# Optimization experiments

Hardware: AMD Instinct MI355X
Metric: run time of the kernel (lower is better)

## Reference

```python
import jax, jax.numpy as jnp
import numpy as np

ATTN_MASK_VALUE = -1e10
HEADS, DIM_HEAD, WSZ = 8, 64, 512


def ln(x, scale, eps=1e-5):
    # haiku LayerNorm(create_scale=True, create_offset=False, axis=-1)
    m = x.mean(-1, keepdims=True)
    v = ((x - m) ** 2).mean(-1, keepdims=True)
    return (x - m) / jnp.sqrt(v + eps) * scale


def local_attn(x, ln_s, qkv_w, ow, ob):
    n, _ = x.shape
    w = n // WSZ
    xn = ln(x, ln_s)
    qkv = xn @ qkv_w                                   # [n, 3*h*d]
    q, k, v = jnp.split(qkv, 3, axis=-1)
    resh = lambda t: t.reshape(w, WSZ, HEADS, DIM_HEAD).transpose(2, 0, 1, 3)  # h w n d
    q, k, v = resh(q), resh(k), resh(v)
    def lookback(t):
        t = jnp.pad(t, ((0, 0), (1, 0), (0, 0), (0, 0)))
        return jnp.concatenate((t[:, :-1], t[:, 1:]), axis=2)  # h w 2*wsz d
    k, v = lookback(k), lookback(v)
    sim = jnp.einsum('hwid,hwjd->hwij', q, k) * (DIM_HEAD ** -0.5)
    mask = jnp.tril(jnp.ones((WSZ, 2 * WSZ), dtype=bool), WSZ)
    sim = jnp.where(mask, sim, ATTN_MASK_VALUE)
    attn = jax.nn.softmax(sim, axis=-1)
    out = jnp.einsum('hwij,hwjd->hwid', attn, v)
    out = out.transpose(1, 2, 0, 3).reshape(n, HEADS * DIM_HEAD)
    return out @ ow + ob


def feedforward(x, ln_s, w1, b1, w2, b2):
    xn = ln(x, ln_s)
    return jax.nn.gelu(xn @ w1 + b1) @ w2 + b2


def gmlp(x, ln_s, win, bin_, sln, sw, sb, sow, sob, pow_, pob):
    n = x.shape[0]
    xn = ln(x, ln_s)
    h = jax.nn.gelu(xn @ win + bin_)                   # [n, d_ff]
    xg, gate = jnp.split(h, 2, axis=-1)                # [n, d_ff/2] each
    gate = ln(gate, sln)
    wm = sw * jnp.tril(jnp.ones((n, n), dtype=sw.dtype))
    gate = jnp.einsum('nd,mn->md', gate, wm) + sb      # causal spatial gate
    s = (xg * gate) @ sow + sob
    return s @ pow_ + pob


def forward(tokens, embed, attn_ln, attn_qkv, attn_ow, attn_ob,
            ff_ln, ff_w1, ff_b1, ff_w2, ff_b2,
            g_ln, g_win, g_bin, g_sln, g_sw, g_sb, g_sow, g_sob, g_pow, g_pob,
            fin_ln, head_w, head_b):
    x = embed[tokens]                                  # [n, dim]

    def block(xc, p):
        xc = xc + local_attn(xc, p['al'], p['aq'], p['aw'], p['ab'])
        xc = xc + feedforward(xc, p['fl'], p['f1'], p['fb1'], p['f2'], p['fb2'])
        return xc, None

    attn_params = {'al': attn_ln, 'aq': attn_qkv, 'aw': attn_ow, 'ab': attn_ob,
                   'fl': ff_ln, 'f1': ff_w1, 'fb1': ff_b1, 'f2': ff_w2, 'fb2': ff_b2}
    x, _ = jax.lax.scan(block, x, attn_params)

    def gblock(xc, p):
        xc = xc + gmlp(xc, p['l'], p['wi'], p['bi'], p['sl'], p['sw'], p['sb'],
                       p['so'], p['sob'], p['po'], p['pob'])
        return xc, None

    g_params = {'l': g_ln, 'wi': g_win, 'bi': g_bin, 'sl': g_sln, 'sw': g_sw,
                'sb': g_sb, 'so': g_sow, 'sob': g_sob, 'po': g_pow, 'pob': g_pob}
    x, _ = jax.lax.scan(gblock, x, g_params)

    return ln(x, fin_ln) @ head_w + head_b             # [n, num_tokens]


def setup_inputs() -> dict:
    key = jax.random.key(0)
    ks = jax.random.split(key, 16)
    n, dim, dff, inner, depth, gdepth, vocab = 2048, 1024, 4096, 512, 6, 2, 32
    sc = 0.02
    eps_sgu = 0.001 / n
    return {
        'tokens': jax.random.randint(ks[0], (n,), 0, vocab),
        'embed': jax.random.normal(ks[1], (vocab, dim)) * sc,
        'attn_ln': jnp.ones((depth, dim)),
        'attn_qkv': jax.random.normal(ks[2], (depth, dim, 3 * inner)) * sc,
        'attn_ow': jax.random.normal(ks[3], (depth, inner, dim)) * sc,
        'attn_ob': jnp.zeros((depth, dim)),
        'ff_ln': jnp.ones((depth, dim)),
        'ff_w1': jax.random.normal(ks[4], (depth, dim, dff)) * sc,
        'ff_b1': jnp.zeros((depth, dff)),
        'ff_w2': jax.random.normal(ks[5], (depth, dff, dim)) * sc,
        'ff_b2': jnp.zeros((depth, dim)),
        'g_ln': jnp.ones((gdepth, dim)),
        'g_win': jax.random.normal(ks[6], (gdepth, dim, dff)) * sc,
        'g_bin': jnp.zeros((gdepth, dff)),
        'g_sln': jnp.ones((gdepth, dff // 2)),
        'g_sw': jax.random.uniform(ks[7], (gdepth, n, n), minval=-eps_sgu, maxval=eps_sgu),
        'g_sb': jnp.ones((gdepth, n, 1)),
        'g_sow': jax.random.normal(ks[8], (gdepth, dff // 2, dff // 2)) * sc,
        'g_sob': jnp.zeros((gdepth, dff // 2)),
        'g_pow': jax.random.normal(ks[9], (gdepth, dff // 2, dim)) * sc,
        'g_pob': jnp.zeros((gdepth, dim)),
        'fin_ln': jnp.ones((dim,)),
        'head_w': jax.random.normal(ks[10], (dim, vocab)) * sc,
        'head_b': jnp.zeros((vocab,)),
    }


def reference(tokens, embed, attn_ln, attn_qkv, attn_ow, attn_ob,
              ff_ln, ff_w1, ff_b1, ff_w2, ff_b2,
              g_ln, g_win, g_bin, g_sln, g_sw, g_sb, g_sow, g_sob, g_pow, g_pob,
              fin_ln, head_w, head_b):
    return forward(tokens, embed, attn_ln, attn_qkv, attn_ow, attn_ob,
                   ff_ln, ff_w1, ff_b1, ff_w2, ff_b2,
                   g_ln, g_win, g_bin, g_sln, g_sw, g_sb, g_sow, g_sob, g_pow, g_pob,
                   fin_ln, head_w, head_b)
```

## Files before the change

kernel.cpp:

```cpp
#include <hip/hip_runtime.h>
#include <hip/hip_bf16.h>
#include <math.h>

using bf16 = __hip_bfloat16;
typedef __bf16 bf16x8 __attribute__((ext_vector_type(8)));
typedef float f32x4 __attribute__((ext_vector_type(4)));

__device__ __forceinline__ float toF(float v) { return v; }
__device__ __forceinline__ float toF(bf16 v) { return __bfloat162float(v); }

__device__ __forceinline__ float gelu_f(float x) {
  float t = tanhf(0.7978845608028654f * (x + 0.044715f * x * x * x));
  return 0.5f * x * (1.0f + t);
}

__device__ __forceinline__ void gld_lds16(const bf16* g, bf16* l) {
  __builtin_amdgcn_global_load_lds(
      (const __attribute__((address_space(1))) void*)g,
      (__attribute__((address_space(3))) void*)l, 16, 0, 0);
}

__device__ __forceinline__ float block_sum(float v) {
  __shared__ float tmp[8];
  int lane = threadIdx.x & 63, w = threadIdx.x >> 6, nw = blockDim.x >> 6;
#pragma unroll
  for (int o = 32; o > 0; o >>= 1) v += __shfl_down(v, o, 64);
  __syncthreads();
  if (lane == 0) tmp[w] = v;
  __syncthreads();
  float r = 0.f;
  for (int i = 0; i < nw; ++i) r += tmp[i];
  return r;
}

__device__ __forceinline__ float block_max(float v) {
  __shared__ float tmp2[8];
  int lane = threadIdx.x & 63, w = threadIdx.x >> 6, nw = blockDim.x >> 6;
#pragma unroll
  for (int o = 32; o > 0; o >>= 1) v = fmaxf(v, __shfl_down(v, o, 64));
  __syncthreads();
  if (lane == 0) tmp2[w] = v;
  __syncthreads();
  float r = -1e30f;
  for (int i = 0; i < nw; ++i) r = fmaxf(r, tmp2[i]);
  return r;
}

template <int BM, int BN, int EPI, int BK, int DBUF>
__launch_bounds__((BM / 64) * (BN / 64) * 64)
__global__ void gemm_bt(const bf16* __restrict__ A, int lda, long sAzh, long sAzw,
                        const bf16* __restrict__ B, int ldb, long sBzh, long sBzw,
                        void* __restrict__ C, int ldc, long sCzh, long sCzw,
                        int M, int N, int K, int zdiv,
                        const float* __restrict__ bias,
                        const float* __restrict__ rowbias,
                        const bf16* __restrict__ mul, int ldmul,
                        float* __restrict__ resid, int trilskip,
                        int nxk, int kchunk) {
  constexpr int LBK = (BK == 64) ? 6 : 5;
  constexpr int WM = BM / 64, WN = BN / 64;
  constexpr int NT = WM * WN * 64;
  constexpr int ACH = (BM * BK) / (NT * 8);
  constexpr int BCH = (BN * BK) / (NT * 8);
  __shared__ __align__(16) bf16 As[(DBUF ? 2 : 1) * BM * BK];
  __shared__ __align__(16) bf16 Bs[(DBUF ? 2 : 1) * BN * BK];
  const int tid = threadIdx.x;
  const int wave = tid >> 6, lane = tid & 63;
  const int wm = wave / WN, wn = wave % WN;
  int bx = blockIdx.x, kc = 0;
  if (kchunk > 0) { kc = bx / nxk; bx -= kc * nxk; }
  const int m0 = blockIdx.y * BM, n0 = bx * BN;
  const int z = blockIdx.z;
  const int zh = z / zdiv, zw = z % zdiv;
  A += zh * sAzh + zw * sAzw;
  B += zh * sBzh + zw * sBzw;
  const long coff = zh * sCzh + zw * sCzw;

  f32x4 acc[4][4];
#pragma unroll
  for (int i = 0; i < 4; ++i)
#pragma unroll
    for (int j = 0; j < 4; ++j)
#pragma unroll
      for (int r = 0; r < 4; ++r) acc[i][j][r] = 0.0f;

  const int kbeg = (kchunk > 0) ? kc * kchunk : 0;
  int kend = K;
  if (kchunk > 0 && kbeg + kchunk < kend) kend = kbeg + kchunk;
  if (trilskip && m0 + BM < kend) kend = m0 + BM;
  const int lrow = lane & 15, lk = (lane >> 4) << 3;

  auto stage = [&](int sel, int k0) {
    bf16* Ad = As + sel * BM * BK;
    bf16* Bd = Bs + sel * BN * BK;
#pragma unroll
    for (int c = 0; c < ACH; ++c) {
      int e = (c * NT + tid) << 3;
      int r = e >> LBK, kk = e & (BK - 1);
      gld_lds16(A + (long)(m0 + r) * lda + (k0 + kk), Ad + e);
    }
#pragma unroll
    for (int c = 0; c < BCH; ++c) {
      int e = (c * NT + tid) << 3;
      int r = e >> LBK, kk = e & (BK - 1);
      gld_lds16(B + (long)(n0 + r) * ldb + (k0 + kk), Bd + e);
    }
  };
  auto zero_diag = [&](int sel, int k0) {
    bf16* Ad = As + sel * BM * BK;
#pragma unroll
    for (int c = 0; c < ACH; ++c) {
      int e = (c * NT + tid) << 3;
      int r = e >> LBK, kk = e & (BK - 1);
      int m = m0 + r;
#pragma unroll
      for (int q = 0; q < 8; ++q)
        if (k0 + kk + q > m) Ad[e + q] = __float2bfloat16(0.0f);
    }
  };
  auto compute = [&](int sel) {
    const bf16* Ad = As + sel * BM * BK;
    const bf16* Bd = Bs + sel * BN * BK;
#pragma unroll
    for (int kk2 = 0; kk2 < BK; kk2 += 32) {
      bf16x8 af[4], bg[4];
#pragma unroll
      for (int i = 0; i < 4; ++i)
        af[i] = *(const bf16x8*)(Ad + (wm * 64 + i * 16 + lrow) * BK + kk2 + lk);
#pragma unroll
      for (int j = 0; j < 4; ++j)
        bg[j] = *(const bf16x8*)(Bd + (wn * 64 + j * 16 + lrow) * BK + kk2 + lk);
#pragma unroll
      for (int i = 0; i < 4; ++i)
#pragma unroll
        for (int j = 0; j < 4; ++j)
          acc[i][j] = __builtin_amdgcn_mfma_f32_16x16x32_bf16(af[i], bg[j], acc[i][j], 0, 0, 0);
    }
  };

  if constexpr (DBUF) {
    int cur = 0;
    stage(0, kbeg);
    __syncthreads();
    for (int k0 = kbeg; k0 < kend; k0 += BK) {
      if (k0 + BK < kend) stage(cur ^ 1, k0 + BK);
      if (trilskip && (k0 + BK > m0)) { zero_diag(cur, k0); __syncthreads(); }
      compute(cur);
      __syncthreads();
      cur ^= 1;
    }
  } else {
    for (int k0 = kbeg; k0 < kend; k0 += BK) {
      stage(0, k0);
      __syncthreads();
      if (trilskip && (k0 + BK > m0)) { zero_diag(0, k0); __syncthreads(); }
      compute(0);
      __syncthreads();
    }
  }

  const int rbase = m0 + wm * 64 + ((lane >> 4) << 2);
  const int cbase = n0 + wn * 64 + (lane & 15);
#pragma unroll
  for (int i = 0; i < 4; ++i) {
#pragma unroll
    for (int j = 0; j < 4; ++j) {
#pragma unroll
      for (int r = 0; r < 4; ++r) {
        int row = rbase + i * 16 + r;
        int col = cbase + j * 16;
        float v = acc[i][j][r];
        long idx = coff + (long)row * ldc + col;
        if (EPI == 0) {
          if (bias) v += bias[col];
          ((bf16*)C)[idx] = __float2bfloat16(v);
        } else if (EPI == 2) {
          v += bias[col];
          ((bf16*)C)[idx] = __float2bfloat16(gelu_f(v));
        } else if (EPI == 3) {
          if (kchunk > 0) {
            if (kbeg == 0 && bias) v += bias[col];
            atomicAdd(&resid[idx], v);
          } else {
            if (bias) v += bias[col];
            resid[idx] += v;
          }
        } else if (EPI == 4) {
          v += rowbias[row];
          v *= __bfloat162float(mul[(long)row * ldmul + col]);
          ((bf16*)C)[idx] = __float2bfloat16(v);
        }
      }
    }
  }
}

__global__ void k_embed(const int* __restrict__ tokens, const float* __restrict__ embed,
                        float* __restrict__ x) {
  int t = blockIdx.x;
  int tok = tokens[t];
  for (int j = threadIdx.x; j < 1024; j += 256)
    x[(long)t * 1024 + j] = embed[(long)tok * 1024 + j];
}

template <typename TIN>
__global__ void k_ln(const TIN* __restrict__ in, int ldin, const float* __restrict__ scale,
                     bf16* __restrict__ out, int ldout, int C) {
  int row = blockIdx.x, tid = threadIdx.x;
  const TIN* p = in + (long)row * ldin;
  float loc[8];
  int nper = C >> 8;
  float s = 0.f;
  for (int c = 0; c < nper; ++c) {
    float v = toF(p[c * 256 + tid]);
    loc[c] = v;
    s += v;
  }
  s = block_sum(s);
  float mean = s / (float)C;
  float s2 = 0.f;
  for (int c = 0; c < nper; ++c) {
    float d = loc[c] - mean;
    s2 += d * d;
  }
  s2 = block_sum(s2);
  float inv = 1.0f / sqrtf(s2 / (float)C + 1e-5f);
  for (int c = 0; c < nper; ++c) {
    int j = c * 256 + tid;
    out[(long)row * ldout + j] = __float2bfloat16((loc[c] - mean) * inv * scale[j]);
  }
}

template <typename TIN>
__global__ void k_transpose(const TIN* __restrict__ in, int ldin, bf16* __restrict__ out,
                            int ldout, int rows, int cols) {
  __shared__ bf16 tile[32][33];
  int c0 = blockIdx.x * 32, r0 = blockIdx.y * 32;
  int tx = threadIdx.x & 31, ty = threadIdx.x >> 5;
#pragma unroll
  for (int j = 0; j < 32; j += 8)
    tile[ty + j][tx] = __float2bfloat16(toF(in[(long)(r0 + ty + j) * ldin + c0 + tx]));
  __syncthreads();
#pragma unroll
  for (int j = 0; j < 32; j += 8)
    out[(long)(c0 + ty + j) * ldout + r0 + tx] = tile[tx][ty + j];
}

__global__ void k_cast(const float* __restrict__ in, bf16* __restrict__ out, long n) {
  long i = (long)blockIdx.x * 256 + threadIdx.x;
  if (i < n) out[i] = __float2bfloat16(in[i]);
}

__global__ void k_zerof(float* __restrict__ p, long n) {
  long i = (long)blockIdx.x * 256 + threadIdx.x;
  if (i < n) p[i] = 0.0f;
}

__global__ void k_packk(const bf16* __restrict__ qkv, bf16* __restrict__ kpad) {
  int idx = blockIdx.x * 256 + threadIdx.x;
  int d = idx & 63, t = (idx >> 6) & 2047, h = idx >> 17;
  kpad[(long)h * 163840 + (512 + t) * 64 + d] = qkv[(long)t * 1536 + 512 + h * 64 + d];
}

__global__ void k_zeropad(bf16* __restrict__ kpad, bf16* __restrict__ vtpad) {
  int idx = blockIdx.x * 256 + threadIdx.x;
  bf16 z = __float2bfloat16(0.0f);
  if (idx < 262144) {
    int h = idx >> 15, off = idx & 32767;
    kpad[(long)h * 163840 + off] = z;
  } else {
    int i = idx - 262144;
    int f = i >> 9, j = i & 511;
    vtpad[(long)f * 2560 + j] = z;
  }
}

__global__ void k_softmax(bf16* __restrict__ SP) {
  int row = blockIdx.x;
  int i = row & 511;
  int limit = i + 513;
  bf16* s = SP + (long)row * 1024;
  int tid = threadIdx.x;
  float v[4];
  float mx = -1e30f;
#pragma unroll
  for (int c = 0; c < 4; ++c) {
    int j = c * 256 + tid;
    float xv = (j < limit) ? __bfloat162float(s[j]) * 0.125f : -1e30f;
    v[c] = xv;
    mx = fmaxf(mx, xv);
  }
  mx = block_max(mx);
  float sum = 0.f;
#pragma unroll
  for (int c = 0; c < 4; ++c) {
    float e = (v[c] <= -1e29f) ? 0.f : expf(v[c] - mx);
    v[c] = e;
    sum += e;
  }
  sum = block_sum(sum);
  float inv = 1.0f / sum;
#pragma unroll
  for (int c = 0; c < 4; ++c) {
    int j = c * 256 + tid;
    s[j] = __float2bfloat16(v[c] * inv);
  }
}

__global__ void k_head(const float* __restrict__ x, const float* __restrict__ sc,
                       const float* __restrict__ w, const float* __restrict__ b,
                       float* __restrict__ out) {
  int row = blockIdx.x, tid = threadIdx.x;
  __shared__ float xn[1024];
  const float* p = x + (long)row * 1024;
  float loc[4];
  float s = 0.f;
#pragma unroll
  for (int c = 0; c < 4; ++c) {
    float v = p[c * 256 + tid];
    loc[c] = v;
    s += v;
  }
  s = block_sum(s);
  float mean = s / 1024.f;
  float s2 = 0.f;
#pragma unroll
  for (int c = 0; c < 4; ++c) {
    float d = loc[c] - mean;
    s2 += d * d;
  }
  s2 = block_sum(s2);
  float inv = 1.0f / sqrtf(s2 / 1024.f + 1e-5f);
#pragma unroll
  for (int c = 0; c < 4; ++c) {
    int j = c * 256 + tid;
    xn[j] = (loc[c] - mean) * inv * sc[j];
  }
  __syncthreads();
  int t = tid & 31, sl = tid >> 5;
  float partial = 0.f;
  for (int kk = 0; kk < 128; ++kk) {
    int k = sl * 128 + kk;
    partial += xn[k] * w[k * 32 + t];
  }
  __shared__ float red[256];
  red[tid] = partial;
  __syncthreads();
  if (tid < 32) {
    float r = 0.f;
    for (int q = 0; q < 8; ++q) r += red[q * 32 + t];
    out[(long)row * 32 + t] = r + b[t];
  }
}

extern "C" void kernel_launch(void* const* d_in, const int* in_sizes, int n_in,
                              void* d_out, int out_size, void* d_ws, size_t ws_size,
                              hipStream_t stream) {
  (void)in_sizes; (void)n_in; (void)out_size; (void)ws_size;
  const int*   tokens   = (const int*)d_in[0];
  const float* embed    = (const float*)d_in[1];
  const float* attn_ln  = (const float*)d_in[2];
  const float* attn_qkv = (const float*)d_in[3];
  const float* attn_ow  = (const float*)d_in[4];
  const float* attn_ob  = (const float*)d_in[5];
  const float* ff_ln    = (const float*)d_in[6];
  const float* ff_w1    = (const float*)d_in[7];
  const float* ff_b1    = (const float*)d_in[8];
  const float* ff_w2    = (const float*)d_in[9];
  const float* ff_b2    = (const float*)d_in[10];
  const float* g_ln     = (const float*)d_in[11];
  const float* g_win    = (const float*)d_in[12];
  const float* g_bin    = (const float*)d_in[13];
  const float* g_sln    = (const float*)d_in[14];
  const float* g_sw     = (const float*)d_in[15];
  const float* g_sb     = (const float*)d_in[16];
  const float* g_sow    = (const float*)d_in[17];
  const float* g_sob    = (const float*)d_in[18];
  const float* g_pow    = (const float*)d_in[19];
  const float* g_pob    = (const float*)d_in[20];
  const float* fin_ln   = (const float*)d_in[21];
  const float* head_w   = (const float*)d_in[22];
  const float* head_b   = (const float*)d_in[23];

  char* ws = (char*)d_ws;
  float* x  = (float*)ws;
  bf16* xn  = (bf16*)(ws + 8388608);
  char* SC  = ws + 12582912;
  bf16* qkv   = (bf16*)SC;
  bf16* kpad  = (bf16*)(SC + 6291456);
  bf16* vtpad = (bf16*)(SC + 8912896);
  bf16* SP    = (bf16*)(SC + 11534336);
  bf16* att   = (bf16*)(SC + 45088768);
  bf16* h      = (bf16*)SC;
  bf16* gateLN = (bf16*)(SC + 16777216);
  bf16* gateT  = (bf16*)(SC + 25165824);
  bf16* prod   = (bf16*)(SC + 33554432);
  bf16* sbuf   = (bf16*)(SC + 41943040);
  bf16* W  = (bf16*)(ws + 62914560);
  bf16* W2 = (bf16*)(ws + 71303168);
  float* att_f32 = (float*)(ws + 71303168);

  k_embed<<<2048, 256, 0, stream>>>(tokens, embed, x);

  for (int L = 0; L < 6; ++L) {
    const float* qkvw = attn_qkv + (long)L * 1024 * 1536;
    const float* oww  = attn_ow + (long)L * 512 * 1024;
    const float* w1   = ff_w1 + (long)L * 1024 * 4096;
    const float* w2   = ff_w2 + (long)L * 4096 * 1024;

    k_ln<float><<<2048, 256, 0, stream>>>(x, 1024, attn_ln + L * 1024, xn, 1024, 1024);
    k_transpose<float><<<dim3(48, 32), 256, 0, stream>>>(qkvw, 1536, W, 1024, 1024, 1536);
    gemm_bt<128, 128, 0, 64, 1><<<dim3(12, 16, 1), 256, 0, stream>>>(
        xn, 1024, 0, 0, W, 1024, 0, 0, qkv, 1536, 0, 0,
        2048, 1536, 1024, 1, nullptr, nullptr, nullptr, 0, nullptr, 0, 0, 0);

    k_packk<<<4096, 256, 0, stream>>>(qkv, kpad);
    k_zeropad<<<2048, 256, 0, stream>>>(kpad, vtpad);
    k_transpose<bf16><<<dim3(16, 64), 256, 0, stream>>>(qkv + 1024, 1536, vtpad + 512, 2560, 2048, 512);

    gemm_bt<128, 128, 0, 64, 0><<<dim3(8, 4, 32), 256, 0, stream>>>(
        qkv, 1536, 64, 786432, kpad, 64, 163840, 32768, SP, 1024, 2097152, 524288,
        512, 1024, 64, 4, nullptr, nullptr, nullptr, 0, nullptr, 0, 0, 0);
    k_softmax<<<16384, 256, 0, stream>>>(SP);
    k_zerof<<<4096, 256, 0, stream>>>(att_f32, 1048576L);
    gemm_bt<128, 64, 3, 64, 1><<<dim3(4, 4, 32), 128, 0, stream>>>(
        SP, 1024, 2097152, 524288, vtpad, 2560, 163840, 512, nullptr, 512, 64, 262144,
        512, 64, 1024, 4, nullptr, nullptr, nullptr, 0, att_f32, 0, 1, 256);
    k_cast<<<4096, 256, 0, stream>>>(att_f32, att, 1048576L);
    k_transpose<float><<<dim3(32, 16), 256, 0, stream>>>(oww, 1024, W, 512, 512, 1024);
    gemm_bt<128, 128, 3, 64, 1><<<dim3(16, 16, 1), 256, 0, stream>>>(
        att, 512, 0, 0, W, 512, 0, 0, nullptr, 1024, 0, 0,
        2048, 1024, 512, 1, attn_ob + L * 1024, nullptr, nullptr, 0, x, 0, 8, 256);

    k_ln<float><<<2048, 256, 0, stream>>>(x, 1024, ff_ln + L * 1024, xn, 1024, 1024);
    k_transpose<float><<<dim3(128, 32), 256, 0, stream>>>(w1, 4096, W, 1024, 1024, 4096);
    gemm_bt<128, 128, 2, 64, 1><<<dim3(32, 16, 1), 256, 0, stream>>>(
        xn, 1024, 0, 0, W, 1024, 0, 0, h, 4096, 0, 0,
        2048, 4096, 1024, 1, ff_b1 + L * 4096, nullptr, nullptr, 0, nullptr, 0, 0, 0);
    k_transpose<float><<<dim3(32, 128), 256, 0, stream>>>(w2, 1024, W, 4096, 4096, 1024);
    gemm_bt<128, 128, 3, 64, 1><<<dim3(32, 16, 1), 256, 0, stream>>>(
        h, 4096, 0, 0, W, 4096, 0, 0, nullptr, 1024, 0, 0,
        2048, 1024, 4096, 1, ff_b2 + L * 1024, nullptr, nullptr, 0, x, 0, 8, 1024);
  }

  for (int G = 0; G < 2; ++G) {
    const float* winw = g_win + (long)G * 1024 * 4096;
    const float* soww = g_sow + (long)G * 2048 * 2048;
    const float* poww = g_pow + (long)G * 2048 * 1024;

    k_ln<float><<<2048, 256, 0, stream>>>(x, 1024, g_ln + G * 1024, xn, 1024, 1024);
    k_transpose<float><<<dim3(128, 32), 256, 0, stream>>>(winw, 4096, W, 1024, 1024, 4096);
    gemm_bt<128, 128, 2, 64, 1><<<dim3(32, 16, 1), 256, 0, stream>>>(
        xn, 1024, 0, 0, W, 1024, 0, 0, h, 4096, 0, 0,
        2048, 4096, 1024, 1, g_bin + G * 4096, nullptr, nullptr, 0, nullptr, 0, 0, 0);
    k_ln<bf16><<<2048, 256, 0, stream>>>(h + 2048, 4096, g_sln + G * 2048, gateLN, 2048, 2048);
    k_transpose<bf16><<<dim3(64, 64), 256, 0, stream>>>(gateLN, 2048, gateT, 2048, 2048, 2048);
    k_cast<<<16384, 256, 0, stream>>>(g_sw + (long)G * 2048 * 2048, W2, 4194304L);
    gemm_bt<128, 128, 4, 64, 1><<<dim3(16, 16, 1), 256, 0, stream>>>(
        W2, 2048, 0, 0, gateT, 2048, 0, 0, prod, 2048, 0, 0,
        2048, 2048, 2048, 1, nullptr, g_sb + G * 2048, h, 4096, nullptr, 1, 0, 0);
    k_transpose<float><<<dim3(64, 64), 256, 0, stream>>>(soww, 2048, W, 2048, 2048, 2048);
    gemm_bt<128, 128, 0, 64, 1><<<dim3(16, 16, 1), 256, 0, stream>>>(
        prod, 2048, 0, 0, W, 2048, 0, 0, sbuf, 2048, 0, 0,
        2048, 2048, 2048, 1, g_sob + G * 2048, nullptr, nullptr, 0, nullptr, 0, 0, 0);
    k_transpose<float><<<dim3(32, 64), 256, 0, stream>>>(poww, 1024, W, 2048, 2048, 1024);
    gemm_bt<128, 128, 3, 64, 1><<<dim3(32, 16, 1), 256, 0, stream>>>(
        sbuf, 2048, 0, 0, W, 2048, 0, 0, nullptr, 1024, 0, 0,
        2048, 1024, 2048, 1, g_pob + G * 1024, nullptr, nullptr, 0, x, 0, 8, 512);
  }

  k_head<<<2048, 256, 0, stream>>>(x, fin_ln, head_w, head_b, (float*)d_out);
}
```

Measured before the change: 2.404 ms.

## Use triple-buffered LDS pipeline with explicit vmcnt waits in GEMM

Replaces the double-buffered GEMM main loop with a three-stage LDS ring: loads are issued two tiles ahead, and partial s_waitcnt vmcnt waits replace full __syncthreads. The aim is to hide global-to-LDS latency by keeping more loads in flight. BK drops from 64 to 32 so three buffers fit in LDS, which doubles the number of loop iterations and barriers. Correctness depends on vmcnt counting matching the number of load instructions issued per stage, and on the barrier plus sched_barrier ordering.

```diff
diff --git a/kernel.cpp b/kernel.cpp
--- a/kernel.cpp
+++ b/kernel.cpp
@@ -20,6 +20,11 @@
       (__attribute__((address_space(3))) void*)l, 16, 0, 0);
 }
 
+template <int N>
+__device__ __forceinline__ void vm_wait() {
+  asm volatile("s_waitcnt vmcnt(%0)" ::"i"(N) : "memory");
+}
+
 __device__ __forceinline__ float block_sum(float v) {
   __shared__ float tmp[8];
   int lane = threadIdx.x & 63, w = threadIdx.x >> 6, nw = blockDim.x >> 6;
@@ -46,7 +51,7 @@
   return r;
 }
 
-template <int BM, int BN, int EPI, int BK, int DBUF>
+template <int BM, int BN, int EPI, int BK>
 __launch_bounds__((BM / 64) * (BN / 64) * 64)
 __global__ void gemm_bt(const bf16* __restrict__ A, int lda, long sAzh, long sAzw,
                         const bf16* __restrict__ B, int ldb, long sBzh, long sBzw,
@@ -62,8 +67,10 @@
   constexpr int NT = WM * WN * 64;
   constexpr int ACH = (BM * BK) / (NT * 8);
   constexpr int BCH = (BN * BK) / (NT * 8);
-  __shared__ __align__(16) bf16 As[(DBUF ? 2 : 1) * BM * BK];
-  __shared__ __align__(16) bf16 Bs[(DBUF ? 2 : 1) * BN * BK];
+  constexpr int S = ACH + BCH;
+  constexpr int NBUF = 3;
+  __shared__ __align__(16) bf16 As[NBUF * BM * BK];
+  __shared__ __align__(16) bf16 Bs[NBUF * BN * BK];
   const int tid = threadIdx.x;
   const int wave = tid >> 6, lane = tid & 63;
   const int wm = wave / WN, wn = wave % WN;
@@ -88,6 +95,7 @@
   int kend = K;
   if (kchunk > 0 && kbeg + kchunk < kend) kend = kbeg + kchunk;
   if (trilskip && m0 + BM < kend) kend = m0 + BM;
+  const int nt = (kend - kbeg) / BK;
   const int lrow = lane & 15, lk = (lane >> 4) << 3;
 
   auto stage = [&](int sel, int k0) {
@@ -138,25 +146,28 @@
     }
   };
 
-  if constexpr (DBUF) {
-    int cur = 0;
-    stage(0, kbeg);
-    __syncthreads();
-    for (int k0 = kbeg; k0 < kend; k0 += BK) {
-      if (k0 + BK < kend) stage(cur ^ 1, k0 + BK);
-      if (trilskip && (k0 + BK > m0)) { zero_diag(cur, k0); __syncthreads(); }
-      compute(cur);
-      __syncthreads();
-      cur ^= 1;
-    }
-  } else {
-    for (int k0 = kbeg; k0 < kend; k0 += BK) {
-      stage(0, k0);
-      __syncthreads();
-      if (trilskip && (k0 + BK > m0)) { zero_diag(0, k0); __syncthreads(); }
-      compute(0);
-      __syncthreads();
-    }
+  stage(0, kbeg);
+  if (nt > 1) stage(1, kbeg + BK);
+  int sel = 0;
+  for (int t = 0; t < nt; ++t) {
+    const int k0 = kbeg + t * BK;
+    if (t + 2 < nt) stage((sel + 2) % NBUF, k0 + 2 * BK);
+    const int ahead = nt - 1 - t;
+    if (ahead >= 2) vm_wait<2 * S>();
+    else if (ahead == 1) vm_wait<S>();
+    else vm_wait<0>();
+    __builtin_amdgcn_sched_barrier(0);
+    __builtin_amdgcn_s_barrier();
+    __builtin_amdgcn_sched_barrier(0);
+    if (trilskip && (k0 + BK > m0)) {
+      zero_diag(sel, k0);
+      __builtin_amdgcn_s_barrier();
+      __builtin_amdgcn_sched_barrier(0);
+    }
+    compute(sel);
+    __builtin_amdgcn_s_barrier();
+    __builtin_amdgcn_sched_barrier(0);
+    sel = (sel + 1) % NBUF;
   }
 
   const int rbase = m0 + wm * 64 + ((lane >> 4) << 2);
@@ -410,7 +421,7 @@
 
     k_ln<float><<<2048, 256, 0, stream>>>(x, 1024, attn_ln + L * 1024, xn, 1024, 1024);
     k_transpose<float><<<dim3(48, 32), 256, 0, stream>>>(qkvw, 1536, W, 1024, 1024, 1536);
-    gemm_bt<128, 128, 0, 64, 1><<<dim3(12, 16, 1), 256, 0, stream>>>(
+    gemm_bt<128, 128, 0, 32><<<dim3(12, 16, 1), 256, 0, stream>>>(
         xn, 1024, 0, 0, W, 1024, 0, 0, qkv, 1536, 0, 0,
         2048, 1536, 1024, 1, nullptr, nullptr, nullptr, 0, nullptr, 0, 0, 0);
 
@@ -418,27 +429,27 @@
     k_zeropad<<<2048, 256, 0, stream>>>(kpad, vtpad);
     k_transpose<bf16><<<dim3(16, 64), 256, 0, stream>>>(qkv + 1024, 1536, vtpad + 512, 2560, 2048, 512);
 
-    gemm_bt<128, 128, 0, 64, 0><<<dim3(8, 4, 32), 256, 0, stream>>>(
+    gemm_bt<128, 128, 0, 32><<<dim3(8, 4, 32), 256, 0, stream>>>(
         qkv, 1536, 64, 786432, kpad, 64, 163840, 32768, SP, 1024, 2097152, 524288,
         512, 1024, 64, 4, nullptr, nullptr, nullptr, 0, nullptr, 0, 0, 0);
     k_softmax<<<16384, 256, 0, stream>>>(SP);
     k_zerof<<<4096, 256, 0, stream>>>(att_f32, 1048576L);
-    gemm_bt<128, 64, 3, 64, 1><<<dim3(4, 4, 32), 128, 0, stream>>>(
+    gemm_bt<128, 64, 3, 32><<<dim3(4, 4, 32), 128, 0, stream>>>(
         SP, 1024, 2097152, 524288, vtpad, 2560, 163840, 512, nullptr, 512, 64, 262144,
         512, 64, 1024, 4, nullptr, nullptr, nullptr, 0, att_f32, 0, 1, 256);
     k_cast<<<4096, 256, 0, stream>>>(att_f32, att, 1048576L);
     k_transpose<float><<<dim3(32, 16), 256, 0, stream>>>(oww, 1024, W, 512, 512, 1024);
-    gemm_bt<128, 128, 3, 64, 1><<<dim3(16, 16, 1), 256, 0, stream>>>(
+    gemm_bt<128, 128, 3, 32><<<dim3(16, 16, 1), 256, 0, stream>>>(
         att, 512, 0, 0, W, 512, 0, 0, nullptr, 1024, 0, 0,
         2048, 1024, 512, 1, attn_ob + L * 1024, nullptr, nullptr, 0, x, 0, 8, 256);
 
     k_ln<float><<<2048, 256, 0, stream>>>(x, 1024, ff_ln + L * 1024, xn, 1024, 1024);
     k_transpose<float><<<dim3(128, 32), 256, 0, stream>>>(w1, 4096, W, 1024, 1024, 4096);
-    gemm_bt<128, 128, 2, 64, 1><<<dim3(32, 16, 1), 256, 0, stream>>>(
+    gemm_bt<128, 128, 2, 32><<<dim3(32, 16, 1), 256, 0, stream>>>(
         xn, 1024, 0, 0, W, 1024, 0, 0, h, 4096, 0, 0,
         2048, 4096, 1024, 1, ff_b1 + L * 4096, nullptr, nullptr, 0, nullptr, 0, 0, 0);
     k_transpose<float><<<dim3(32, 128), 256, 0, stream>>>(w2, 1024, W, 4096, 4096, 1024);
-    gemm_bt<128, 128, 3, 64, 1><<<dim3(32, 16, 1), 256, 0, stream>>>(
+    gemm_bt<128, 128, 3, 32><<<dim3(32, 16, 1), 256, 0, stream>>>(
         h, 4096, 0, 0, W, 4096, 0, 0, nullptr, 1024, 0, 0,
         2048, 1024, 4096, 1, ff_b2 + L * 1024, nullptr, nullptr, 0, x, 0, 8, 1024);
   }
@@ -450,21 +461,21 @@
 
     k_ln<float><<<2048, 256, 0, stream>>>(x, 1024, g_ln + G * 1024, xn, 1024, 1024);
     k_transpose<float><<<dim3(128, 32), 256, 0, stream>>>(winw, 4096, W, 1024, 1024, 4096);
-    gemm_bt<128, 128, 2, 64, 1><<<dim3(32, 16, 1), 256, 0, stream>>>(
+    gemm_bt<128, 128, 2, 32><<<dim3(32, 16, 1), 256, 0, stream>>>(
         xn, 1024, 0, 0, W, 1024, 0, 0, h, 4096, 0, 0,
         2048, 4096, 1024, 1, g_bin + G * 4096, nullptr, nullptr, 0, nullptr, 0, 0, 0);
     k_ln<bf16><<<2048, 256, 0, stream>>>(h + 2048, 4096, g_sln + G * 2048, gateLN, 2048, 2048);
     k_transpose<bf16><<<dim3(64, 64), 256, 0, stream>>>(gateLN, 2048, gateT, 2048, 2048, 2048);
     k_cast<<<16384, 256, 0, stream>>>(g_sw + (long)G * 2048 * 2048, W2, 4194304L);
-    gemm_bt<128, 128, 4, 64, 1><<<dim3(16, 16, 1), 256, 0, stream>>>(
+    gemm_bt<128, 128, 4, 32><<<dim3(16, 16, 1), 256, 0, stream>>>(
         W2, 2048, 0, 0, gateT, 2048, 0, 0, prod, 2048, 0, 0,
         2048, 2048, 2048, 1, nullptr, g_sb + G * 2048, h, 4096, nullptr, 1, 0, 0);
     k_transpose<float><<<dim3(64, 64), 256, 0, stream>>>(soww, 2048, W, 2048, 2048, 2048);
-    gemm_bt<128, 128, 0, 64, 1><<<dim3(16, 16, 1), 256, 0, stream>>>(
+    gemm_bt<128, 128, 0, 32><<<dim3(16, 16, 1), 256, 0, stream>>>(
         prod, 2048, 0, 0, W, 2048, 0, 0, sbuf, 2048, 0, 0,
         2048, 2048, 2048, 1, g_sob + G * 2048, nullptr, nullptr, 0, nullptr, 0, 0, 0);
     k_transpose<float><<<dim3(32, 64), 256, 0, stream>>>(poww, 1024, W, 2048, 2048, 1024);
-    gemm_bt<128, 128, 3, 64, 1><<<dim3(32, 16, 1), 256, 0, stream>>>(
+    gemm_bt<128, 128, 3, 32><<<dim3(32, 16, 1), 256, 0, stream>>>(
         sbuf, 2048, 0, 0, W, 2048, 0, 0, nullptr, 1024, 0, 0,
         2048, 1024, 2048, 1, g_pob + G * 1024, nullptr, nullptr, 0, x, 0, 8, 512);
   }
```

Result: no change. 2.362 ms (-1.7%).
